# Kernel tuning notes

Measured on AMD Instinct MI355X. Metric: run time of the kernel, lower is better.

## Reference

```python
import jax, jax.numpy as jnp
import numpy as np

N, H, E, ED = 50000, 128, 600000, 32
LN_EPS = 1e-5


def _mlp(x, W1, b1, W2, b2):
    h = jax.nn.gelu(x @ W1 + b1, approximate=False)
    return h @ W2 + b2


def setup_inputs() -> dict:
    key = jax.random.key(0)
    ks = jax.random.split(key, 12)
    s = lambda fan_in: 1.0 / np.sqrt(fan_in)
    return {
        "x": jax.random.normal(ks[0], (N, H), dtype=jnp.float32),
        "edge_index": jax.random.randint(ks[1], (2, E), 0, N, dtype=jnp.int64),
        "edge_attr": jax.random.normal(ks[2], (E, ED), dtype=jnp.float32),
        "eW1": jax.random.normal(ks[3], (2 * H + ED, H), dtype=jnp.float32) * s(2 * H + ED),
        "eb1": jnp.zeros((H,), dtype=jnp.float32),
        "eW2": jax.random.normal(ks[4], (H, H), dtype=jnp.float32) * s(H),
        "eb2": jnp.zeros((H,), dtype=jnp.float32),
        "nW1": jax.random.normal(ks[5], (2 * H, H), dtype=jnp.float32) * s(2 * H),
        "nb1": jnp.zeros((H,), dtype=jnp.float32),
        "nW2": jax.random.normal(ks[6], (H, H), dtype=jnp.float32) * s(H),
        "nb2": jnp.zeros((H,), dtype=jnp.float32),
        "ln_g": jnp.ones((H,), dtype=jnp.float32),
        "ln_b": jnp.zeros((H,), dtype=jnp.float32),
    }


def reference(x, edge_index, edge_attr, eW1, eb1, eW2, eb2, nW1, nb1, nW2, nb2, ln_g, ln_b):
    src, dst = edge_index[0], edge_index[1]
    # edge MLP on gathered endpoint features + edge attrs: [E, 2H+ED] -> [E, H]
    msg = _mlp(jnp.concatenate([x[src], x[dst], edge_attr], axis=-1), eW1, eb1, eW2, eb2)
    # scatter-mean into destination nodes
    agg = jax.ops.segment_sum(msg, dst, num_segments=x.shape[0])
    count = jax.ops.segment_sum(jnp.ones((dst.shape[0], 1), dtype=x.dtype), dst, num_segments=x.shape[0])
    agg = agg / (count + 1e-8)
    # node MLP + residual + layernorm
    out = _mlp(jnp.concatenate([x, agg], axis=-1), nW1, nb1, nW2, nb2) + x
    mu = jnp.mean(out, axis=-1, keepdims=True)
    var = jnp.mean(jnp.square(out - mu), axis=-1, keepdims=True)
    return (out - mu) * jax.lax.rsqrt(var + LN_EPS) * ln_g + ln_b
```

## Files before the change

### kernel.cpp

```cpp
#include <hip/hip_runtime.h>
#include <hip/hip_fp16.h>
#include <math.h>

#define NN 50000
#define HH 128
#define EE 600000
#define EDD 32
#define NBINS 50176
#define NPRE 782
#define NWG_E (EE / 64)

typedef __attribute__((ext_vector_type(8))) _Float16 half8;
typedef __attribute__((ext_vector_type(4))) float f32x4;

__device__ __forceinline__ unsigned pkh(float a, float b) {
  __half2 h = __floats2half2_rn(a, b);
  return *reinterpret_cast<unsigned*>(&h);
}
__device__ __forceinline__ unsigned hadd2u(unsigned a, unsigned b) {
  __half2 x = *reinterpret_cast<__half2*>(&a);
  __half2 y = *reinterpret_cast<__half2*>(&b);
  __half2 s = __hadd2(x, y);
  return *reinterpret_cast<unsigned*>(&s);
}
__device__ __forceinline__ unsigned hmul2u(unsigned a, unsigned b) {
  __half2 x = *reinterpret_cast<__half2*>(&a);
  __half2 y = *reinterpret_cast<__half2*>(&b);
  __half2 s = __hmul2(x, y);
  return *reinterpret_cast<unsigned*>(&s);
}
__device__ __forceinline__ float lo16f(unsigned u) {
  __half2 h = *reinterpret_cast<__half2*>(&u);
  return __low2float(h);
}
__device__ __forceinline__ float hi16f(unsigned u) {
  __half2 h = *reinterpret_cast<__half2*>(&u);
  return __high2float(h);
}
__device__ __forceinline__ short f2hs(float f) {
  __half h = __float2half_rn(f);
  return *reinterpret_cast<short*>(&h);
}
__device__ __forceinline__ float h2f(short s) {
  __half h = *reinterpret_cast<__half*>(&s);
  return __half2float(h);
}

__device__ __forceinline__ float gelu_f(float v) {
  float u = 2.3022082f * v * fmaf(0.044715f, v * v, 1.0f);
  float e = __builtin_amdgcn_exp2f(u);
  float r = __builtin_amdgcn_rcpf(e + 1.0f);
  return fmaf(-v, r, v);
}

#define FS 132
__global__ __launch_bounds__(256) void k_setup(
    const float* __restrict__ eW1, const float* __restrict__ nW1,
    const float* __restrict__ nW2, const float* __restrict__ eW2,
    const float* __restrict__ eb2, const long long* __restrict__ ei,
    long long nmax,
    short* __restrict__ pe1, short* __restrict__ pn1, short* __restrict__ pn2,
    short* __restrict__ pnW2p, float* __restrict__ b2p,
    int* __restrict__ zbase, int* __restrict__ flag) {
  __shared__ short sA[64 * 136];
  __shared__ float sR[64 * FS];
  __shared__ int bad;
  const int blk = blockIdx.x;
  const int tid = threadIdx.x;

  if (blk < 42) {
    const int b = blk * 4 + (tid >> 6);
    const int l = tid & 63;
    const float* W;
    short* P;
    int bb;
    if (b < 72)       { W = eW1; P = pe1; bb = b; }
    else if (b < 136) { W = nW1; P = pn1; bb = b - 72; }
    else              { W = nW2; P = pn2; bb = b - 136; }
    const int kt = bb >> 3, ct = bb & 7;
    short v[8];
#pragma unroll
    for (int j = 0; j < 8; ++j)
      v[j] = f2hs(W[(size_t)(kt * 32 + ((l >> 4) * 8 + j)) * HH + ct * 16 + (l & 15)]);
    short* dst = P + ((size_t)bb * 64 + l) * 8;
#pragma unroll
    for (int j = 0; j < 8; ++j) dst[j] = v[j];
    return;
  }
  if (blk == 42) {
    if (tid == 0) bad = 0;
    __syncthreads();
    for (int i = tid; i < 2048; i += 256) {
      long long v = ei[i];
      if (v < 0 || v >= nmax) bad = 1;
    }
    __syncthreads();
    if (tid == 0) *flag = (bad ? 0 : 1);
    return;
  }
  if (blk < 92) {
    int idx = (blk - 43) * 2048 + tid * 8;
    int4 z = {0, 0, 0, 0};
    *(int4*)(zbase + idx) = z;
    *(int4*)(zbase + idx + 4) = z;
    return;
  }
  if (blk == 94) {
    if (tid < 128) {
      float acc = 0.f;
#pragma unroll 4
      for (int k = 0; k < 128; ++k)
        acc += eb2[k] * nW1[(size_t)(128 + k) * HH + tid];
      b2p[tid] = acc;
    }
    return;
  }
  {
    const int b = blk - 92;
    const int le = tid >> 2, lq = tid & 3;
    const int wv = tid >> 6, l = tid & 63, lr = l & 15, kq = l >> 4;

    half8 bf[8];
#pragma unroll
    for (int kt = 0; kt < 4; ++kt)
#pragma unroll
      for (int c = 0; c < 2; ++c) {
        half8 v;
#pragma unroll
        for (int j = 0; j < 8; ++j)
          v[j] = (_Float16)nW1[(size_t)(128 + kt * 32 + ((l >> 4) * 8 + j)) * HH +
                               (wv * 2 + c) * 16 + (l & 15)];
        bf[kt * 2 + c] = v;
      }
    {
      const float4* xs = (const float4*)(eW2 + (size_t)(64 * b + le) * HH);
#pragma unroll
      for (int i = 0; i < 4; ++i) {
        float4 a = xs[lq * 8 + i * 2], c = xs[lq * 8 + i * 2 + 1];
        uint4 u = {pkh(a.x, a.y), pkh(a.z, a.w), pkh(c.x, c.y), pkh(c.z, c.w)};
        *(uint4*)&sA[le * 136 + lq * 32 + i * 8] = u;
      }
    }
    __syncthreads();

    f32x4 acc[4][2];
    const f32x4 zero = {0.f, 0.f, 0.f, 0.f};
#pragma unroll
    for (int m = 0; m < 4; ++m) { acc[m][0] = zero; acc[m][1] = zero; }
    const short* ab = &sA[lr * 136 + kq * 8];
#pragma unroll
    for (int kt = 0; kt < 4; ++kt) {
      half8 af[4];
#pragma unroll
      for (int m = 0; m < 4; ++m) af[m] = *(const half8*)(ab + m * 16 * 136 + kt * 32);
#pragma unroll
      for (int m = 0; m < 4; ++m)
#pragma unroll
        for (int c = 0; c < 2; ++c)
          acc[m][c] = __builtin_amdgcn_mfma_f32_16x16x32_f16(af[m], bf[kt * 2 + c], acc[m][c], 0, 0, 0);
    }
#pragma unroll
    for (int c = 0; c < 2; ++c)
#pragma unroll
      for (int m = 0; m < 4; ++m)
#pragma unroll
        for (int r = 0; r < 4; ++r)
          sR[(m * 16 + kq * 4 + r) * FS + wv * 32 + c * 16 + lr] = acc[m][c][r];
    __syncthreads();

#pragma unroll
    for (int it = 0; it < 4; ++it) {
      int item = tid + 256 * it;
      int lane = item & 63;
      int pair = item >> 6;
      int ktl = pair >> 3, ct = pair & 7;
      short v[8];
#pragma unroll
      for (int j = 0; j < 8; ++j) {
        int kpos = ktl * 32 + ((lane >> 4) * 8 + j);
        int t2 = kpos >> 1, h2 = kpos & 1;
        int rowl = (t2 >> 4) * 32 + (t2 & 15) + 16 * h2;
        int colp = ct * 16 + (lane & 15);
        v[j] = f2hs(sR[rowl * FS + colp]);
      }
      short* dst = pnW2p + (((size_t)(2 * b + ktl) * 8 + ct) * 64 + lane) * 8;
#pragma unroll
      for (int j = 0; j < 8; ++j) dst[j] = v[j];
    }
  }
}

__global__ __launch_bounds__(256, 4) void k_preh(
    const float* __restrict__ x, const short* __restrict__ pW1,
    const void* __restrict__ eiv, const int* __restrict__ flag,
    unsigned* __restrict__ Psw, unsigned* __restrict__ Pdw,
    unsigned* __restrict__ HaggH2, int* __restrict__ chist) {
  __shared__ short sX[64 * 136];
  const int blk = blockIdx.x;
  const int tid = threadIdx.x;

  if (blk >= NPRE) {
    int e = (blk - NPRE) * 256 + tid;
    if (e < EE) {
      int d;
      if (*flag) d = (int)((const long long*)eiv)[EE + e];
      else       d = ((const int*)eiv)[EE + e];
      atomicAdd(&chist[d], 1);
    }
    return;
  }

  const int r0 = blk * 64;
  const int le = tid >> 2, lq = tid & 3;
  const int wv = tid >> 6, l = tid & 63, lr = l & 15, kq = l >> 4;

  {
    int gr = r0 + le;
    if (gr < NN) {
      uint4 z = {0, 0, 0, 0};
      uint4* hp = (uint4*)(HaggH2 + (size_t)gr * 64);
#pragma unroll
      for (int i = 0; i < 4; ++i) hp[lq * 4 + i] = z;
    }
  }

  const half8* bp = (const half8*)pW1;
  half8 fa[8], fb[8];
#pragma unroll
  for (int kt = 0; kt < 4; ++kt)
#pragma unroll
    for (int c = 0; c < 2; ++c) {
      fa[kt * 2 + c] = bp[(kt * 8 + wv * 2 + c) * 64 + l];
      fb[kt * 2 + c] = bp[((kt + 4) * 8 + wv * 2 + c) * 64 + l];
    }
  {
    int gr = r0 + le;
    if (gr < NN) {
      const float4* xs = (const float4*)(x + (size_t)gr * HH);
#pragma unroll
      for (int i = 0; i < 4; ++i) {
        float4 a = xs[lq * 8 + i * 2], c = xs[lq * 8 + i * 2 + 1];
        uint4 u = {pkh(a.x, a.y), pkh(a.z, a.w), pkh(c.x, c.y), pkh(c.z, c.w)};
        *(uint4*)&sX[le * 136 + lq * 32 + i * 8] = u;
      }
    } else {
      uint4 z = {0, 0, 0, 0};
#pragma unroll
      for (int i = 0; i < 4; ++i) *(uint4*)&sX[le * 136 + lq * 32 + i * 8] = z;
    }
  }
  __syncthreads();

  f32x4 as_[4][2], ad[4][2];
  const f32x4 zero = {0.f, 0.f, 0.f, 0.f};
#pragma unroll
  for (int m = 0; m < 4; ++m) { as_[m][0] = zero; as_[m][1] = zero; ad[m][0] = zero; ad[m][1] = zero; }
  const short* ab = &sX[lr * 136 + kq * 8];
#pragma unroll
  for (int kt = 0; kt < 4; ++kt) {
    half8 af[4];
#pragma unroll
    for (int m = 0; m < 4; ++m) af[m] = *(const half8*)(ab + m * 16 * 136 + kt * 32);
#pragma unroll
    for (int m = 0; m < 4; ++m)
#pragma unroll
      for (int c = 0; c < 2; ++c) {
        as_[m][c] = __builtin_amdgcn_mfma_f32_16x16x32_f16(af[m], fa[kt * 2 + c], as_[m][c], 0, 0, 0);
        ad[m][c] = __builtin_amdgcn_mfma_f32_16x16x32_f16(af[m], fb[kt * 2 + c], ad[m][c], 0, 0, 0);
      }
  }
#pragma unroll
  for (int m = 0; m < 4; ++m)
#pragma unroll
    for (int r = 0; r < 4; ++r) {
      int grow = r0 + m * 16 + kq * 4 + r;
      if (grow < NN) {
        Psw[(size_t)grow * 64 + wv * 16 + lr] = pkh(as_[m][0][r], as_[m][1][r]);
        Pdw[(size_t)grow * 64 + wv * 16 + lr] = pkh(ad[m][0][r], ad[m][1][r]);
      }
    }
}

__global__ void k_scan1(const int* __restrict__ chist, int* __restrict__ tmp,
                        int* __restrict__ bsum) {
  __shared__ int buf[2][256];
  int t = threadIdx.x;
  int i = blockIdx.x * 256 + t;
  buf[0][t] = chist[i];
  __syncthreads();
  int cur = 0;
  for (int o = 1; o < 256; o <<= 1) {
    int v = buf[cur][t];
    if (t >= o) v += buf[cur][t - o];
    buf[cur ^ 1][t] = v;
    __syncthreads();
    cur ^= 1;
  }
  tmp[i] = buf[cur][t];
  if (t == 255) bsum[blockIdx.x] = buf[cur][255];
}

__global__ void k_scatter(const void* __restrict__ eiv, const int* __restrict__ flag,
                          const int* __restrict__ tmp, const int* __restrict__ chist,
                          const int* __restrict__ bsum, int* __restrict__ cntW,
                          unsigned long long* __restrict__ e8) {
  __shared__ int sB[2][256];
  const int t = threadIdx.x;
  int orig = (t < 196) ? bsum[t] : 0;
  sB[0][t] = orig;
  __syncthreads();
  int cur = 0;
  for (int o = 1; o < 256; o <<= 1) {
    int v = sB[cur][t];
    if (t >= o) v += sB[cur][t - o];
    sB[cur ^ 1][t] = v;
    __syncthreads();
    cur ^= 1;
  }
  sB[1][t] = sB[0][t] - orig;
  __syncthreads();

  int e = blockIdx.x * 256 + t;
  if (e >= EE) return;
  int s, d;
  if (*flag) {
    const long long* p = (const long long*)eiv;
    s = (int)p[e];
    d = (int)p[EE + e];
  } else {
    const int* p = (const int*)eiv;
    s = p[e];
    d = p[EE + e];
  }
  int base = tmp[d] - chist[d] + sB[1][d >> 8];
  int pos = base + atomicAdd(&cntW[d], 1);
  e8[pos] = (unsigned long long)s | ((unsigned long long)d << 20) |
            ((unsigned long long)e << 40);
}

#define SFP 68
__global__ __launch_bounds__(256, 7) void k_edge(
    const unsigned* __restrict__ Psw, const unsigned* __restrict__ Pdw,
    const float* __restrict__ ea,
    const short* __restrict__ pW1, const float* __restrict__ b1,
    const unsigned long long* __restrict__ e8, unsigned* __restrict__ HaggH2) {
  __shared__ unsigned sFp[64 * SFP];
  __shared__ short sEA[64 * 40];
  __shared__ int sDst[64];

  int orig = blockIdx.x;
  const int q8 = NWG_E >> 3, r8 = NWG_E & 7;
  int xcd = orig & 7, lid = orig >> 3;
  int swz = (xcd < r8) ? xcd * (q8 + 1) + lid
                       : r8 * (q8 + 1) + (xcd - r8) * q8 + lid;

  const int tid = threadIdx.x;
  const int e0 = swz * 64;
  const int le = tid >> 2, lq = tid & 3;
  const int wv = tid >> 6, l = tid & 63, lr = l & 15, kq = l >> 4;

  half8 w1c[2];
#pragma unroll
  for (int c = 0; c < 2; ++c)
    w1c[c] = ((const half8*)pW1)[(64 + wv * 2 + c) * 64 + l];

  const unsigned long long er = e8[e0 + le];
  const int gs = (int)(er & 0xFFFFF);
  const int gd = (int)((er >> 20) & 0xFFFFF);
  const int ge = (int)(er >> 40);
  if (lq == 0) sDst[le] = gd;

  {
    const uint4* ps = (const uint4*)(Psw + (size_t)gs * 64);
    const uint4* pd = (const uint4*)(Pdw + (size_t)gd * 64);
#pragma unroll
    for (int i = 0; i < 4; ++i) {
      uint4 a = ps[lq * 4 + i];
      uint4 b = pd[lq * 4 + i];
      uint4 s = {hadd2u(a.x, b.x), hadd2u(a.y, b.y), hadd2u(a.z, b.z), hadd2u(a.w, b.w)};
      *(uint4*)&sFp[le * SFP + lq * 16 + i * 4] = s;
    }
    const float4* ep = (const float4*)(ea + (size_t)ge * EDD);
    float4 a = ep[lq * 2], b = ep[lq * 2 + 1];
    uint4 u = {pkh(a.x, a.y), pkh(a.z, a.w), pkh(b.x, b.y), pkh(b.z, b.w)};
    *(uint4*)&sEA[le * 40 + lq * 8] = u;
  }
  __syncthreads();

  f32x4 acc[4][2];
  const f32x4 zero = {0.f, 0.f, 0.f, 0.f};
#pragma unroll
  for (int m = 0; m < 4; ++m) { acc[m][0] = zero; acc[m][1] = zero; }
  {
#pragma unroll
    for (int m = 0; m < 4; ++m) {
      half8 af = *(const half8*)&sEA[(m * 16 + lr) * 40 + kq * 8];
#pragma unroll
      for (int c = 0; c < 2; ++c)
        acc[m][c] = __builtin_amdgcn_mfma_f32_16x16x32_f16(af, w1c[c], acc[m][c], 0, 0, 0);
    }
  }

  const float b1c0 = b1[wv * 32 + lr];
  const float b1c1 = b1[wv * 32 + 16 + lr];
  unsigned pr[4][4];
#pragma unroll
  for (int m = 0; m < 4; ++m)
#pragma unroll
    for (int r = 0; r < 4; ++r) {
      const int row = m * 16 + kq * 4 + r;
      unsigned up = sFp[row * SFP + wv * 16 + lr];
      float v0 = acc[m][0][r] + lo16f(up) + b1c0;
      float v1 = acc[m][1][r] + hi16f(up) + b1c1;
      pr[m][r] = pkh(gelu_f(v0), gelu_f(v1));
    }
  __syncthreads();

  {
    unsigned* tp = &sFp[(wv * 16 + lr) * SFP];
#pragma unroll
    for (int m = 0; m < 4; ++m) {
      uint4 u = {pr[m][0], pr[m][1], pr[m][2], pr[m][3]};
      *(uint4*)&tp[m * 16 + kq * 4] = u;
    }
  }
  __syncthreads();

  {
    const int p = tid & 63;
    const int q = tid >> 6;
    const unsigned* tp2 = &sFp[p * SFP + q * 16];
    const int rend = q * 16 + 15;
    float r0s = 0.f, r1s = 0.f;
#pragma unroll
    for (int i = 0; i < 4; ++i) {
      uint4 u4 = *(const uint4*)&tp2[i * 4];
      unsigned uu[4] = {u4.x, u4.y, u4.z, u4.w};
#pragma unroll
      for (int j = 0; j < 4; ++j) {
        int r = q * 16 + i * 4 + j;
        r0s += lo16f(uu[j]);
        r1s += hi16f(uu[j]);
        int dcur = sDst[r];
        bool last = (r == rend) || (sDst[r + 1] != dcur);
        if (last) {
          unsafeAtomicAdd((__half2*)&HaggH2[(size_t)dcur * 64 + p],
                          __floats2half2_rn(r0s, r1s));
          r0s = 0.f;
          r1s = 0.f;
        }
      }
    }
  }
}

#define NS 264
__global__ __launch_bounds__(256, 4) void k_node(
    const float* __restrict__ x,
    const unsigned* __restrict__ HaggH2, const int* __restrict__ chist,
    const short* __restrict__ pn1, const short* __restrict__ pnW2p,
    const float* __restrict__ nb1, const float* __restrict__ b2p,
    const short* __restrict__ pn2, const float* __restrict__ nb2,
    const float* __restrict__ g, const float* __restrict__ be,
    float* __restrict__ out) {
  __shared__ short sA[64 * NS];
  __shared__ float sP[64 * 4];
  __shared__ float sP2[64 * 4];
  __shared__ float sFac[64];

  const int tid = threadIdx.x;
  const int r0 = blockIdx.x * 64;
  const int le = tid >> 2;
  const int lq = tid & 3;
  const int wv = tid >> 6;
  const int l = tid & 63;
  const int lr = l & 15;
  const int kq = l >> 4;

  const half8* bpa = (const half8*)pn1;
  const half8* bpc = (const half8*)pnW2p;
  half8 b1f[16];
#pragma unroll
  for (int kt = 0; kt < 4; ++kt)
#pragma unroll
    for (int c = 0; c < 2; ++c) {
      b1f[kt * 2 + c] = bpa[(kt * 8 + wv * 2 + c) * 64 + l];
      b1f[(kt + 4) * 2 + c] = bpc[(kt * 8 + wv * 2 + c) * 64 + l];
    }

  {
    const int gr = r0 + le;
    short* row = &sA[le * NS];
    if (gr < NN) {
      float cntf = (float)chist[gr];
      float rinv = 1.0f / (cntf + 1e-8f);
      if (lq == 0) sFac[le] = cntf * rinv;
      const float4* xs = (const float4*)(x + (size_t)gr * HH);
#pragma unroll
      for (int i = 0; i < 4; ++i) {
        float4 a = xs[lq * 8 + i * 2], c = xs[lq * 8 + i * 2 + 1];
        uint4 u = {pkh(a.x, a.y), pkh(a.z, a.w), pkh(c.x, c.y), pkh(c.z, c.w)};
        *(uint4*)(row + lq * 32 + i * 8) = u;
      }
      const unsigned rv2 = pkh(rinv, rinv);
      const uint4* hs = (const uint4*)(HaggH2 + (size_t)gr * 64);
#pragma unroll
      for (int i = 0; i < 4; ++i) {
        uint4 u = hs[lq * 4 + i];
        u.x = hmul2u(u.x, rv2);
        u.y = hmul2u(u.y, rv2);
        u.z = hmul2u(u.z, rv2);
        u.w = hmul2u(u.w, rv2);
        *(uint4*)(row + 128 + lq * 32 + i * 8) = u;
      }
    } else {
      if (lq == 0) sFac[le] = 0.f;
      uint4 z = {0, 0, 0, 0};
#pragma unroll
      for (int i = 0; i < 8; ++i) *(uint4*)(row + lq * 64 + i * 8) = z;
    }
  }
  __syncthreads();

  f32x4 acc[4][2];
  const f32x4 zero = {0.f, 0.f, 0.f, 0.f};
#pragma unroll
  for (int m = 0; m < 4; ++m) { acc[m][0] = zero; acc[m][1] = zero; }
  const short* ab = &sA[lr * NS + kq * 8];
#pragma unroll
  for (int kt = 0; kt < 8; ++kt) {
    half8 af[4];
#pragma unroll
    for (int m = 0; m < 4; ++m)
      af[m] = *(const half8*)(ab + m * 16 * NS + kt * 32);
#pragma unroll
    for (int m = 0; m < 4; ++m)
#pragma unroll
      for (int c = 0; c < 2; ++c)
        acc[m][c] = __builtin_amdgcn_mfma_f32_16x16x32_f16(af[m], b1f[kt * 2 + c], acc[m][c], 0, 0, 0);
  }

  const half8* bp2 = (const half8*)pn2;
  half8 b2f_[8];
#pragma unroll
  for (int kt = 0; kt < 4; ++kt)
#pragma unroll
    for (int c = 0; c < 2; ++c)
      b2f_[kt * 2 + c] = bp2[(kt * 8 + wv * 2 + c) * 64 + l];

  __syncthreads();

#pragma unroll
  for (int c = 0; c < 2; ++c) {
    const int col = wv * 32 + c * 16 + lr;
    const float b1v = nb1[col];
    const float b2pv = b2p[col];
#pragma unroll
    for (int m = 0; m < 4; ++m)
#pragma unroll
      for (int r = 0; r < 4; ++r) {
        const int row = m * 16 + kq * 4 + r;
        float fac = sFac[row];
        sA[row * NS + 128 + col] = f2hs(gelu_f(acc[m][c][r] + b1v + fac * b2pv));
      }
  }
  __syncthreads();

  f32x4 acc2[4][2];
#pragma unroll
  for (int m = 0; m < 4; ++m) { acc2[m][0] = zero; acc2[m][1] = zero; }
#pragma unroll
  for (int kt = 0; kt < 4; ++kt) {
    half8 af[4];
#pragma unroll
    for (int m = 0; m < 4; ++m)
      af[m] = *(const half8*)(ab + m * 16 * NS + 128 + kt * 32);
#pragma unroll
    for (int m = 0; m < 4; ++m)
#pragma unroll
      for (int c = 0; c < 2; ++c)
        acc2[m][c] = __builtin_amdgcn_mfma_f32_16x16x32_f16(af[m], b2f_[kt * 2 + c], acc2[m][c], 0, 0, 0);
  }

  float val[4][2][4];
#pragma unroll
  for (int c = 0; c < 2; ++c) {
    const int col = wv * 32 + c * 16 + lr;
    const float b2v = nb2[col];
#pragma unroll
    for (int m = 0; m < 4; ++m)
#pragma unroll
      for (int r = 0; r < 4; ++r) {
        const int lrow = m * 16 + kq * 4 + r;
        float xr = h2f(sA[lrow * NS + col]);
        val[m][c][r] = acc2[m][c][r] + b2v + xr;
      }
  }
#pragma unroll
  for (int m = 0; m < 4; ++m)
#pragma unroll
    for (int r = 0; r < 4; ++r) {
      float s = val[m][0][r] + val[m][1][r];
      float s2 = val[m][0][r] * val[m][0][r] + val[m][1][r] * val[m][1][r];
#pragma unroll
      for (int o = 1; o < 16; o <<= 1) {
        s += __shfl_xor(s, o);
        s2 += __shfl_xor(s2, o);
      }
      if (lr == 0) {
        const int row = m * 16 + kq * 4 + r;
        sP[row * 4 + wv] = s;
        sP2[row * 4 + wv] = s2;
      }
    }
  __syncthreads();

#pragma unroll
  for (int c = 0; c < 2; ++c) {
    const int col = wv * 32 + c * 16 + lr;
    const float gv = g[col];
    const float bv = be[col];
#pragma unroll
    for (int m = 0; m < 4; ++m)
#pragma unroll
      for (int r = 0; r < 4; ++r) {
        const int lrow = m * 16 + kq * 4 + r;
        const int row = r0 + lrow;
        if (row < NN) {
          float4 ps = *(float4*)&sP[lrow * 4];
          float4 qs = *(float4*)&sP2[lrow * 4];
          float s = ps.x + ps.y + ps.z + ps.w;
          float s2 = qs.x + qs.y + qs.z + qs.w;
          float mu = s * 0.0078125f;
          float var = s2 * 0.0078125f - mu * mu;
          float rs = rsqrtf(var + 1e-5f);
          out[(size_t)row * HH + col] = (val[m][c][r] - mu) * rs * gv + bv;
        }
      }
  }
}

extern "C" void kernel_launch(void* const* d_in, const int* in_sizes, int n_in,
                              void* d_out, int out_size, void* d_ws, size_t ws_size,
                              hipStream_t stream) {
  const float* x = (const float*)d_in[0];
  const void* ei = d_in[1];
  const float* ea = (const float*)d_in[2];
  const float* eW1 = (const float*)d_in[3];
  const float* eb1 = (const float*)d_in[4];
  const float* eW2 = (const float*)d_in[5];
  const float* eb2 = (const float*)d_in[6];
  const float* nW1 = (const float*)d_in[7];
  const float* nb1 = (const float*)d_in[8];
  const float* nW2 = (const float*)d_in[9];
  const float* nb2 = (const float*)d_in[10];
  const float* lng = (const float*)d_in[11];
  const float* lnb = (const float*)d_in[12];
  float* out = (float*)d_out;

  char* w = (char*)d_ws;
  size_t off = 0;
  auto alloc = [&](size_t bytes) { void* p = w + off; off = (off + bytes + 255) & ~(size_t)255; return p; };
  unsigned* HaggH2 = (unsigned*)alloc((size_t)NN * 64 * 4);
  int* chist = (int*)alloc((size_t)NBINS * 4);
  int* cntW = (int*)alloc((size_t)NBINS * 4);
  short* pe1 = (short*)alloc((size_t)72 * 512 * 2);
  short* pn1 = (short*)alloc((size_t)64 * 512 * 2);
  short* pn2 = (short*)alloc((size_t)32 * 512 * 2);
  short* pnW2p = (short*)alloc((size_t)32 * 512 * 2);
  float* b2p = (float*)alloc(HH * 4);
  unsigned long long* e8 = (unsigned long long*)alloc((size_t)EE * 8);
  int* tmpS = (int*)alloc((size_t)NBINS * 4);
  int* bsum = (int*)alloc(256 * 4);
  int* flag = (int*)alloc(256);
  unsigned* Psw = (unsigned*)alloc((size_t)NN * 64 * 4);
  unsigned* Pdw = (unsigned*)alloc((size_t)NN * 64 * 4);

  k_setup<<<95, 256, 0, stream>>>(eW1, nW1, nW2, eW2, eb2, (const long long*)ei,
                                  (long long)NN, pe1, pn1, pn2, pnW2p, b2p, chist, flag);
  k_preh<<<NPRE + (EE + 255) / 256, 256, 0, stream>>>(x, pe1, ei, flag, Psw, Pdw, HaggH2, chist);
  k_scan1<<<NBINS / 256, 256, 0, stream>>>(chist, tmpS, bsum);
  k_scatter<<<(EE + 255) / 256, 256, 0, stream>>>(ei, flag, tmpS, chist, bsum, cntW, e8);
  k_edge<<<NWG_E, 256, 0, stream>>>(Psw, Pdw, ea, pe1, eb1, e8, HaggH2);
  k_node<<<(NN + 63) / 64, 256, 0, stream>>>(x, HaggH2, chist, pn1, pnW2p, nb1, b2p, pn2, nb2, lng, lnb, out);
}
```

Baseline: 156.4 us.

## Fold edge bias into precompute, memset zeroing, and batch histogram atomics

```diff
diff --git a/kernel.cpp b/kernel.cpp
--- a/kernel.cpp
+++ b/kernel.cpp
@@ -8,6 +8,7 @@
 #define EDD 32
 #define NBINS 50176
 #define NPRE 782
+#define NHIST 586
 #define NWG_E (EE / 64)
 
 typedef __attribute__((ext_vector_type(8))) _Float16 half8;
@@ -47,7 +48,7 @@
 }
 
 __device__ __forceinline__ float gelu_f(float v) {
-  float u = 2.3022082f * v * fmaf(0.044715f, v * v, 1.0f);
+  float u = v * fmaf(0.10294324f, v * v, 2.3022082f);
   float e = __builtin_amdgcn_exp2f(u);
   float r = __builtin_amdgcn_rcpf(e + 1.0f);
   return fmaf(-v, r, v);
@@ -60,8 +61,7 @@
     const float* __restrict__ eb2, const long long* __restrict__ ei,
     long long nmax,
     short* __restrict__ pe1, short* __restrict__ pn1, short* __restrict__ pn2,
-    short* __restrict__ pnW2p, float* __restrict__ b2p,
-    int* __restrict__ zbase, int* __restrict__ flag) {
+    short* __restrict__ pnW2p, float* __restrict__ b2p, int* __restrict__ flag) {
   __shared__ short sA[64 * 136];
   __shared__ float sR[64 * FS];
   __shared__ int bad;
@@ -98,14 +98,7 @@
     if (tid == 0) *flag = (bad ? 0 : 1);
     return;
   }
-  if (blk < 92) {
-    int idx = (blk - 43) * 2048 + tid * 8;
-    int4 z = {0, 0, 0, 0};
-    *(int4*)(zbase + idx) = z;
-    *(int4*)(zbase + idx + 4) = z;
-    return;
-  }
-  if (blk == 94) {
+  if (blk == 45) {
     if (tid < 128) {
       float acc = 0.f;
 #pragma unroll 4
@@ -116,7 +109,7 @@
     return;
   }
   {
-    const int b = blk - 92;
+    const int b = blk - 43;
     const int le = tid >> 2, lq = tid & 3;
     const int wv = tid >> 6, l = tid & 63, lr = l & 15, kq = l >> 4;
 
@@ -192,20 +185,37 @@
 
 __global__ __launch_bounds__(256, 4) void k_preh(
     const float* __restrict__ x, const short* __restrict__ pW1,
+    const float* __restrict__ eb1,
     const void* __restrict__ eiv, const int* __restrict__ flag,
     unsigned* __restrict__ Psw, unsigned* __restrict__ Pdw,
-    unsigned* __restrict__ HaggH2, int* __restrict__ chist) {
+    int* __restrict__ chist) {
   __shared__ short sX[64 * 136];
   const int blk = blockIdx.x;
   const int tid = threadIdx.x;
 
   if (blk >= NPRE) {
-    int e = (blk - NPRE) * 256 + tid;
-    if (e < EE) {
-      int d;
-      if (*flag) d = (int)((const long long*)eiv)[EE + e];
-      else       d = ((const int*)eiv)[EE + e];
-      atomicAdd(&chist[d], 1);
+    int base = ((blk - NPRE) * 256 + tid) * 4;
+    if (*flag) {
+      const long long* p = (const long long*)eiv + EE;
+#pragma unroll
+      for (int j = 0; j < 4; ++j) {
+        int e = base + j;
+        if (e < EE) atomicAdd(&chist[(int)p[e]], 1);
+      }
+    } else {
+      const int* p = (const int*)eiv + EE;
+      if (base + 3 < EE) {
+        int4 d4 = *(const int4*)(p + base);
+        atomicAdd(&chist[d4.x], 1);
+        atomicAdd(&chist[d4.y], 1);
+        atomicAdd(&chist[d4.z], 1);
+        atomicAdd(&chist[d4.w], 1);
+      } else {
+        for (int j = 0; j < 4; ++j) {
+          int e = base + j;
+          if (e < EE) atomicAdd(&chist[p[e]], 1);
+        }
+      }
     }
     return;
   }
@@ -214,15 +224,8 @@
   const int le = tid >> 2, lq = tid & 3;
   const int wv = tid >> 6, l = tid & 63, lr = l & 15, kq = l >> 4;
 
-  {
-    int gr = r0 + le;
-    if (gr < NN) {
-      uint4 z = {0, 0, 0, 0};
-      uint4* hp = (uint4*)(HaggH2 + (size_t)gr * 64);
-#pragma unroll
-      for (int i = 0; i < 4; ++i) hp[lq * 4 + i] = z;
-    }
-  }
+  const float b1c0 = eb1[wv * 32 + lr];
+  const float b1c1 = eb1[wv * 32 + 16 + lr];
 
   const half8* bp = (const half8*)pW1;
   half8 fa[8], fb[8];
@@ -275,7 +278,8 @@
     for (int r = 0; r < 4; ++r) {
       int grow = r0 + m * 16 + kq * 4 + r;
       if (grow < NN) {
-        Psw[(size_t)grow * 64 + wv * 16 + lr] = pkh(as_[m][0][r], as_[m][1][r]);
+        Psw[(size_t)grow * 64 + wv * 16 + lr] =
+            pkh(as_[m][0][r] + b1c0, as_[m][1][r] + b1c1);
         Pdw[(size_t)grow * 64 + wv * 16 + lr] = pkh(ad[m][0][r], ad[m][1][r]);
       }
     }
@@ -342,7 +346,7 @@
 __global__ __launch_bounds__(256, 7) void k_edge(
     const unsigned* __restrict__ Psw, const unsigned* __restrict__ Pdw,
     const float* __restrict__ ea,
-    const short* __restrict__ pW1, const float* __restrict__ b1,
+    const short* __restrict__ pW1,
     const unsigned long long* __restrict__ e8, unsigned* __restrict__ HaggH2) {
   __shared__ unsigned sFp[64 * SFP];
   __shared__ short sEA[64 * 40];
@@ -401,8 +405,6 @@
     }
   }
 
-  const float b1c0 = b1[wv * 32 + lr];
-  const float b1c1 = b1[wv * 32 + 16 + lr];
   unsigned pr[4][4];
 #pragma unroll
   for (int m = 0; m < 4; ++m)
@@ -410,8 +412,8 @@
     for (int r = 0; r < 4; ++r) {
       const int row = m * 16 + kq * 4 + r;
       unsigned up = sFp[row * SFP + wv * 16 + lr];
-      float v0 = acc[m][0][r] + lo16f(up) + b1c0;
-      float v1 = acc[m][1][r] + hi16f(up) + b1c1;
+      float v0 = acc[m][0][r] + lo16f(up);
+      float v1 = acc[m][1][r] + hi16f(up);
       pr[m][r] = pkh(gelu_f(v0), gelu_f(v1));
     }
   __syncthreads();
@@ -676,11 +678,12 @@
   unsigned* Psw = (unsigned*)alloc((size_t)NN * 64 * 4);
   unsigned* Pdw = (unsigned*)alloc((size_t)NN * 64 * 4);
 
-  k_setup<<<95, 256, 0, stream>>>(eW1, nW1, nW2, eW2, eb2, (const long long*)ei,
-                                  (long long)NN, pe1, pn1, pn2, pnW2p, b2p, chist, flag);
-  k_preh<<<NPRE + (EE + 255) / 256, 256, 0, stream>>>(x, pe1, ei, flag, Psw, Pdw, HaggH2, chist);
+  hipMemsetAsync(HaggH2, 0, (size_t)NN * 64 * 4 + (size_t)NBINS * 4 * 2, stream);
+  k_setup<<<46, 256, 0, stream>>>(eW1, nW1, nW2, eW2, eb2, (const long long*)ei,
+                                  (long long)NN, pe1, pn1, pn2, pnW2p, b2p, flag);
+  k_preh<<<NPRE + NHIST, 256, 0, stream>>>(x, pe1, eb1, ei, flag, Psw, Pdw, chist);
   k_scan1<<<NBINS / 256, 256, 0, stream>>>(chist, tmpS, bsum);
   k_scatter<<<(EE + 255) / 256, 256, 0, stream>>>(ei, flag, tmpS, chist, bsum, cntW, e8);
-  k_edge<<<NWG_E, 256, 0, stream>>>(Psw, Pdw, ea, pe1, eb1, e8, HaggH2);
+  k_edge<<<NWG_E, 256, 0, stream>>>(Psw, Pdw, ea, pe1, e8, HaggH2);
   k_node<<<(NN + 63) / 64, 256, 0, stream>>>(x, HaggH2, chist, pn1, pnW2p, nb1, b2p, pn2, nb2, lng, lnb, out);
 }
```

Measured after the change: 157.6 us. No clear change (+0.8%).
